# Optimization experiments

Measured on AMD Instinct MI355X. Metric: run time of the kernel, lower is better.

## Reference

```python
import jax, jax.numpy as jnp
import numpy as np

# Channel layout assumed by the model's CH dict
CH_ELEV, CH_WS, CH_WD, CH_HUM, CH_NDVI, CH_FIRE = 0, 1, 2, 3, 4, 5
P_BURN, W_WIND, W_SLOPE = 0.58, 0.045, 0.078
OFFSETS = [(-1, 0), (-1, 1), (0, 1), (1, 1), (1, 0), (1, -1), (0, -1), (-1, -1)]
DIR_ANGLES = [90.0, 45.0, 0.0, 315.0, 270.0, 225.0, 180.0, 135.0]
SOBEL_X = np.array([[-1, 0, 1], [-2, 0, 2], [-1, 0, 1]], np.float32) / 8.0
SOBEL_Y = np.array([[-1, -2, -1], [0, 0, 0], [1, 2, 1]], np.float32) / 8.0


def setup_inputs() -> dict:
    key = jax.random.key(0)
    x = jax.random.uniform(key, (16, 6, 1024, 1024), dtype=jnp.float32)
    return {"x": x}


def _conv2d_same(img, k):
    # img: (B,1,H,W), k: (3,3)
    kern = jnp.asarray(k).reshape(1, 1, 3, 3)
    return jax.lax.conv_general_dilated(img, kern, (1, 1), ((1, 1), (1, 1)))


def _shift(mask, dr, dc):
    # mask: (B,H,W) float; zero-padded shift matching torch slicing
    B, H, W = mask.shape
    p = jnp.pad(mask, ((0, 0), (1, 1), (1, 1)))
    return p[:, 1 + dr:1 + dr + H, 1 + dc:1 + dc + W]


def reference(x):
    B, C, H, W = x.shape
    elev = x[:, CH_ELEV:CH_ELEV + 1]          # (B,1,H,W)
    ws = x[:, CH_WS]                           # (B,H,W)
    wd = x[:, CH_WD]
    hum = x[:, CH_HUM]
    ndvi = x[:, CH_NDVI]
    fs = x[:, CH_FIRE]

    dx = _conv2d_same(elev, SOBEL_X)
    dy = _conv2d_same(elev, SOBEL_Y)
    grad_mag = jnp.sqrt(dx * dx + dy * dy + 1e-8)
    slope = (jnp.arctan(grad_mag) * (180.0 / np.pi))[:, 0]  # (B,H,W) degrees

    burning = (fs > 0.5).astype(x.dtype)
    wind_math = jnp.mod(270.0 - wd, 360.0)
    slope_effect = 1.0 + W_SLOPE * jnp.tan(slope * (np.pi / 180.0))
    moisture_damp = jnp.clip(1.0 - 2.0 * hum * 200.0, 0.3, 1.0)
    veg_factor = 0.5 + 0.5 * jnp.clip(ndvi, 0.0, 1.0)
    base = P_BURN * slope_effect * moisture_damp * veg_factor  # wind-independent part

    prob = jnp.zeros((B, H, W), dtype=x.dtype)
    for (dr, dc), d_angle in zip(OFFSETS, DIR_ANGLES):
        shifted = _shift(burning, dr, dc)
        angle_diff = (d_angle - wind_math) * (np.pi / 180.0)
        wind_factor = 1.0 + W_WIND * jnp.cos(angle_diff) * ws
        p_spread = jnp.clip(base * wind_factor, 0.0, 1.0)
        prob = jnp.maximum(prob, shifted * p_spread)

    unburned = (fs < 0.5).astype(x.dtype)
    out = jnp.maximum(fs, prob * unburned)
    return out[:, None]  # (B,1,H,W)
```

## Files before the change

### kernel.cpp

```cpp
#include <hip/hip_runtime.h>

namespace {
constexpr int CH = 6;
constexpr int H  = 1024;
constexpr int W  = 1024;
constexpr float P_BURN  = 0.58f;
constexpr float W_WIND  = 0.045f;
constexpr float W_SLOPE = 0.078f;
constexpr float C45     = 0.70710678118654752f;
constexpr float DEG2RAD = 0.017453292519943295f;

__device__ __forceinline__ void load6(const float* __restrict__ plane, int row,
                                      int j0, float v[6]) {
    if ((unsigned)row >= (unsigned)H) {
        v[0] = v[1] = v[2] = v[3] = v[4] = v[5] = 0.f;
        return;
    }
    const float* r = plane + (size_t)row * W;
    const float4 m = *reinterpret_cast<const float4*>(r + j0);
    v[0] = (j0 > 0)     ? r[j0 - 1] : 0.f;
    v[1] = m.x; v[2] = m.y; v[3] = m.z; v[4] = m.w;
    v[5] = (j0 + 4 < W) ? r[j0 + 4] : 0.f;
}
}

__global__ __launch_bounds__(256)
void fire_step(const float* __restrict__ x, float* __restrict__ out, int B) {
    const int nblk  = gridDim.x;
    const int chunk = nblk >> 3;
    const int bid   = blockIdx.x;
    const int srow  = (bid & 7) * chunk + (bid >> 3);

    const int b = srow / H;
    const int i = srow % H;
    if (b >= B) return;
    const int j0 = (int)threadIdx.x * 4;

    const size_t plane = (size_t)H * W;
    const float* base_b = x + (size_t)b * CH * plane;
    const float* elev  = base_b + 0 * plane;
    const float* wsp   = base_b + 1 * plane;
    const float* wdp   = base_b + 2 * plane;
    const float* hump  = base_b + 3 * plane;
    const float* ndvip = base_b + 4 * plane;
    const float* fsp   = base_b + 5 * plane;

    float em[6], ec[6], ep[6];
    load6(elev, i - 1, j0, em);
    load6(elev, i,     j0, ec);
    load6(elev, i + 1, j0, ep);
    float fm[6], fc[6], fq[6];
    load6(fsp, i - 1, j0, fm);
    load6(fsp, i,     j0, fc);
    load6(fsp, i + 1, j0, fq);

    const size_t roff = (size_t)i * W + j0;
    const float4 ws4 = *reinterpret_cast<const float4*>(wsp   + roff);
    const float4 wd4 = *reinterpret_cast<const float4*>(wdp   + roff);
    const float4 hu4 = *reinterpret_cast<const float4*>(hump  + roff);
    const float4 nd4 = *reinterpret_cast<const float4*>(ndvip + roff);
    const float* wsa = reinterpret_cast<const float*>(&ws4);
    const float* wda = reinterpret_cast<const float*>(&wd4);
    const float* hua = reinterpret_cast<const float*>(&hu4);
    const float* nda = reinterpret_cast<const float*>(&nd4);

    float o[4];
#pragma unroll
    for (int k = 0; k < 4; ++k) {
        const float dx = ((em[k+2] - em[k]) + 2.f * (ec[k+2] - ec[k]) +
                          (ep[k+2] - ep[k])) * 0.125f;
        const float dy = ((ep[k]   - em[k]) + 2.f * (ep[k+1] - em[k+1]) +
                          (ep[k+2] - em[k+2])) * 0.125f;
        const float g = sqrtf(dx * dx + dy * dy + 1e-8f);
        const float slope_eff = 1.f + W_SLOPE * g;
        const float moist = fminf(fmaxf(1.f - 400.f * hua[k], 0.3f), 1.f);
        const float veg   = 0.5f + 0.5f * fminf(fmaxf(nda[k], 0.f), 1.f);
        const float basep = P_BURN * slope_eff * moist * veg;

        const float wrad = (270.f - wda[k]) * DEG2RAD;
        float sw, cw;
        __sincosf(wrad, &sw, &cw);

        float best = -2.f;
        if (fm[k+1] > 0.5f) best = fmaxf(best,  sw);
        if (fm[k+2] > 0.5f) best = fmaxf(best,  C45 * (cw + sw));
        if (fc[k+2] > 0.5f) best = fmaxf(best,  cw);
        if (fq[k+2] > 0.5f) best = fmaxf(best,  C45 * (cw - sw));
        if (fq[k+1] > 0.5f) best = fmaxf(best, -sw);
        if (fq[k]   > 0.5f) best = fmaxf(best, -C45 * (cw + sw));
        if (fc[k]   > 0.5f) best = fmaxf(best, -cw);
        if (fm[k]   > 0.5f) best = fmaxf(best,  C45 * (sw - cw));

        float prob = 0.f;
        if (best > -1.5f) {
            const float wf = 1.f + W_WIND * best * wsa[k];
            prob = fminf(fmaxf(basep * wf, 0.f), 1.f);
        }
        const float fsc = fc[k + 1];
        o[k] = fmaxf(fsc, (fsc < 0.5f) ? prob : 0.f);
    }

    float4 ov;
    ov.x = o[0]; ov.y = o[1]; ov.z = o[2]; ov.w = o[3];
    *reinterpret_cast<float4*>(out + (size_t)b * plane + roff) = ov;
}

extern "C" void kernel_launch(void* const* d_in, const int* in_sizes, int n_in,
                              void* d_out, int out_size, void* d_ws, size_t ws_size,
                              hipStream_t stream) {
    const float* x = (const float*)d_in[0];
    float* out = (float*)d_out;
    const int B = in_sizes[0] / (CH * H * W);
    const int blocks = B * H;
    fire_step<<<blocks, 256, 0, stream>>>(x, out, B);
}
```

Measured before the change: 541.3 us.

## Tile elevation and fire planes into shared memory with 2D blocks

Replaces the one-row-per-block layout with 128x16 2D tiles. The elevation and fire-state halos are staged once in LDS and the 3x3 neighbourhoods are read from there, instead of each thread issuing redundant global loads for the neighbouring rows. It also drops the XCD-aware row swizzle. In exchange it adds a __syncthreads, halo overhead of 18 rows per 16 output rows, and about 20 KB of LDS per block, which may limit occupancy.

```diff
diff --git a/kernel.cpp b/kernel.cpp
--- a/kernel.cpp
+++ b/kernel.cpp
@@ -4,105 +4,143 @@
 constexpr int CH = 6;
 constexpr int H  = 1024;
 constexpr int W  = 1024;
+constexpr int TW = 128;
+constexpr int TH = 16;
+constexpr int LW = TW + 8;
+constexpr int LH = TH + 2;
 constexpr float P_BURN  = 0.58f;
 constexpr float W_WIND  = 0.045f;
 constexpr float W_SLOPE = 0.078f;
 constexpr float C45     = 0.70710678118654752f;
 constexpr float DEG2RAD = 0.017453292519943295f;
-
-__device__ __forceinline__ void load6(const float* __restrict__ plane, int row,
-                                      int j0, float v[6]) {
-    if ((unsigned)row >= (unsigned)H) {
-        v[0] = v[1] = v[2] = v[3] = v[4] = v[5] = 0.f;
-        return;
-    }
-    const float* r = plane + (size_t)row * W;
-    const float4 m = *reinterpret_cast<const float4*>(r + j0);
-    v[0] = (j0 > 0)     ? r[j0 - 1] : 0.f;
-    v[1] = m.x; v[2] = m.y; v[3] = m.z; v[4] = m.w;
-    v[5] = (j0 + 4 < W) ? r[j0 + 4] : 0.f;
-}
 }
 
 __global__ __launch_bounds__(256)
 void fire_step(const float* __restrict__ x, float* __restrict__ out, int B) {
-    const int nblk  = gridDim.x;
-    const int chunk = nblk >> 3;
-    const int bid   = blockIdx.x;
-    const int srow  = (bid & 7) * chunk + (bid >> 3);
+    __shared__ float es[LH][LW];
+    __shared__ float fs[LH][LW];
 
-    const int b = srow / H;
-    const int i = srow % H;
+    constexpr int tilesX = W / TW;
+    constexpr int tilesY = H / TH;
+    constexpr int tpi    = tilesX * tilesY;
+
+    const int b  = blockIdx.x / tpi;
+    const int t  = blockIdx.x % tpi;
+    const int r0 = (t / tilesX) * TH;
+    const int c0 = (t % tilesX) * TW;
     if (b >= B) return;
-    const int j0 = (int)threadIdx.x * 4;
 
     const size_t plane = (size_t)H * W;
-    const float* base_b = x + (size_t)b * CH * plane;
-    const float* elev  = base_b + 0 * plane;
-    const float* wsp   = base_b + 1 * plane;
-    const float* wdp   = base_b + 2 * plane;
-    const float* hump  = base_b + 3 * plane;
-    const float* ndvip = base_b + 4 * plane;
-    const float* fsp   = base_b + 5 * plane;
+    const float* bb    = x + (size_t)b * CH * plane;
+    const float* elev  = bb + 0 * plane;
+    const float* wsp   = bb + 1 * plane;
+    const float* wdp   = bb + 2 * plane;
+    const float* hup   = bb + 3 * plane;
+    const float* ndp   = bb + 4 * plane;
+    const float* fsp   = bb + 5 * plane;
 
-    float em[6], ec[6], ep[6];
-    load6(elev, i - 1, j0, em);
-    load6(elev, i,     j0, ec);
-    load6(elev, i + 1, j0, ep);
-    float fm[6], fc[6], fq[6];
-    load6(fsp, i - 1, j0, fm);
-    load6(fsp, i,     j0, fc);
-    load6(fsp, i + 1, j0, fq);
+    for (int idx = threadIdx.x; idx < LH * (LW / 4); idx += 256) {
+        const int lr = idx / (LW / 4);
+        const int g  = idx % (LW / 4);
+        const int gr = r0 - 1 + lr;
+        const int gc = c0 - 4 + 4 * g;
+        float4 e = {0.f, 0.f, 0.f, 0.f};
+        float4 f = {0.f, 0.f, 0.f, 0.f};
+        if ((unsigned)gr < (unsigned)H) {
+            const float* er = elev + (size_t)gr * W;
+            const float* fr = fsp  + (size_t)gr * W;
+            if (gc >= 0 && gc + 3 < W) {
+                e = *reinterpret_cast<const float4*>(er + gc);
+                f = *reinterpret_cast<const float4*>(fr + gc);
+            } else {
+                float* ep_ = reinterpret_cast<float*>(&e);
+                float* fp_ = reinterpret_cast<float*>(&f);
+#pragma unroll
+                for (int k = 0; k < 4; ++k) {
+                    const int c = gc + k;
+                    if ((unsigned)c < (unsigned)W) { ep_[k] = er[c]; fp_[k] = fr[c]; }
+                }
+            }
+        }
+        *reinterpret_cast<float4*>(&es[lr][4 * g]) = e;
+        *reinterpret_cast<float4*>(&fs[lr][4 * g]) = f;
+    }
+    __syncthreads();
 
-    const size_t roff = (size_t)i * W + j0;
-    const float4 ws4 = *reinterpret_cast<const float4*>(wsp   + roff);
-    const float4 wd4 = *reinterpret_cast<const float4*>(wdp   + roff);
-    const float4 hu4 = *reinterpret_cast<const float4*>(hump  + roff);
-    const float4 nd4 = *reinterpret_cast<const float4*>(ndvip + roff);
-    const float* wsa = reinterpret_cast<const float*>(&ws4);
-    const float* wda = reinterpret_cast<const float*>(&wd4);
-    const float* hua = reinterpret_cast<const float*>(&hu4);
-    const float* nda = reinterpret_cast<const float*>(&nd4);
+    const int tx = threadIdx.x & 31;
+    const int ty = threadIdx.x >> 5;
+    const int cbase = 4 * tx + 4;
 
-    float o[4];
+    auto rd6 = [&](const float (*sm)[LW], int r, float v[6]) {
+        const float4 mid = *reinterpret_cast<const float4*>(&sm[r][cbase]);
+        v[0] = sm[r][cbase - 1];
+        v[1] = mid.x; v[2] = mid.y; v[3] = mid.z; v[4] = mid.w;
+        v[5] = sm[r][cbase + 4];
+    };
+
 #pragma unroll
-    for (int k = 0; k < 4; ++k) {
-        const float dx = ((em[k+2] - em[k]) + 2.f * (ec[k+2] - ec[k]) +
-                          (ep[k+2] - ep[k])) * 0.125f;
-        const float dy = ((ep[k]   - em[k]) + 2.f * (ep[k+1] - em[k+1]) +
-                          (ep[k+2] - em[k+2])) * 0.125f;
-        const float g = sqrtf(dx * dx + dy * dy + 1e-8f);
-        const float slope_eff = 1.f + W_SLOPE * g;
-        const float moist = fminf(fmaxf(1.f - 400.f * hua[k], 0.3f), 1.f);
-        const float veg   = 0.5f + 0.5f * fminf(fmaxf(nda[k], 0.f), 1.f);
-        const float basep = P_BURN * slope_eff * moist * veg;
+    for (int s = 0; s < 2; ++s) {
+        const int lr = ty + 8 * s;
+        const int i  = r0 + lr;
+        const size_t roff = (size_t)i * W + c0 + 4 * tx;
 
-        const float wrad = (270.f - wda[k]) * DEG2RAD;
-        float sw, cw;
-        __sincosf(wrad, &sw, &cw);
+        const float4 ws4 = *reinterpret_cast<const float4*>(wsp + roff);
+        const float4 wd4 = *reinterpret_cast<const float4*>(wdp + roff);
+        const float4 hu4 = *reinterpret_cast<const float4*>(hup + roff);
+        const float4 nd4 = *reinterpret_cast<const float4*>(ndp + roff);
+        const float* wsa = reinterpret_cast<const float*>(&ws4);
+        const float* wda = reinterpret_cast<const float*>(&wd4);
+        const float* hua = reinterpret_cast<const float*>(&hu4);
+        const float* nda = reinterpret_cast<const float*>(&nd4);
 
-        float best = -2.f;
-        if (fm[k+1] > 0.5f) best = fmaxf(best,  sw);
-        if (fm[k+2] > 0.5f) best = fmaxf(best,  C45 * (cw + sw));
-        if (fc[k+2] > 0.5f) best = fmaxf(best,  cw);
-        if (fq[k+2] > 0.5f) best = fmaxf(best,  C45 * (cw - sw));
-        if (fq[k+1] > 0.5f) best = fmaxf(best, -sw);
-        if (fq[k]   > 0.5f) best = fmaxf(best, -C45 * (cw + sw));
-        if (fc[k]   > 0.5f) best = fmaxf(best, -cw);
-        if (fm[k]   > 0.5f) best = fmaxf(best,  C45 * (sw - cw));
+        float em[6], ec[6], ep[6], fm[6], fc[6], fq[6];
+        rd6(es, lr,     em);
+        rd6(es, lr + 1, ec);
+        rd6(es, lr + 2, ep);
+        rd6(fs, lr,     fm);
+        rd6(fs, lr + 1, fc);
+        rd6(fs, lr + 2, fq);
 
-        float prob = 0.f;
-        if (best > -1.5f) {
-            const float wf = 1.f + W_WIND * best * wsa[k];
-            prob = fminf(fmaxf(basep * wf, 0.f), 1.f);
+        float o[4];
+#pragma unroll
+        for (int k = 0; k < 4; ++k) {
+            const float dx = ((em[k+2] - em[k]) + 2.f * (ec[k+2] - ec[k]) +
+                              (ep[k+2] - ep[k])) * 0.125f;
+            const float dy = ((ep[k]   - em[k]) + 2.f * (ep[k+1] - em[k+1]) +
+                              (ep[k+2] - em[k+2])) * 0.125f;
+            const float g = sqrtf(dx * dx + dy * dy + 1e-8f);
+            const float slope_eff = 1.f + W_SLOPE * g;
+            const float moist = fminf(fmaxf(1.f - 400.f * hua[k], 0.3f), 1.f);
+            const float veg   = 0.5f + 0.5f * fminf(fmaxf(nda[k], 0.f), 1.f);
+            const float basep = P_BURN * slope_eff * moist * veg;
+
+            const float wrad = (270.f - wda[k]) * DEG2RAD;
+            float sw, cw;
+            __sincosf(wrad, &sw, &cw);
+
+            float best = -2.f;
+            if (fm[k+1] > 0.5f) best = fmaxf(best,  sw);
+            if (fm[k+2] > 0.5f) best = fmaxf(best,  C45 * (cw + sw));
+            if (fc[k+2] > 0.5f) best = fmaxf(best,  cw);
+            if (fq[k+2] > 0.5f) best = fmaxf(best,  C45 * (cw - sw));
+            if (fq[k+1] > 0.5f) best = fmaxf(best, -sw);
+            if (fq[k]   > 0.5f) best = fmaxf(best, -C45 * (cw + sw));
+            if (fc[k]   > 0.5f) best = fmaxf(best, -cw);
+            if (fm[k]   > 0.5f) best = fmaxf(best,  C45 * (sw - cw));
+
+            float prob = 0.f;
+            if (best > -1.5f) {
+                const float wf = 1.f + W_WIND * best * wsa[k];
+                prob = fminf(fmaxf(basep * wf, 0.f), 1.f);
+            }
+            const float fsc = fc[k + 1];
+            o[k] = fmaxf(fsc, (fsc < 0.5f) ? prob : 0.f);
         }
-        const float fsc = fc[k + 1];
-        o[k] = fmaxf(fsc, (fsc < 0.5f) ? prob : 0.f);
+
+        float4 ov;
+        ov.x = o[0]; ov.y = o[1]; ov.z = o[2]; ov.w = o[3];
+        *reinterpret_cast<float4*>(out + (size_t)b * plane + roff) = ov;
     }
-
-    float4 ov;
-    ov.x = o[0]; ov.y = o[1]; ov.z = o[2]; ov.w = o[3];
-    *reinterpret_cast<float4*>(out + (size_t)b * plane + roff) = ov;
 }
 
 extern "C" void kernel_launch(void* const* d_in, const int* in_sizes, int n_in,
@@ -111,6 +149,6 @@
     const float* x = (const float*)d_in[0];
     float* out = (float*)d_out;
     const int B = in_sizes[0] / (CH * H * W);
-    const int blocks = B * H;
+    const int blocks = B * (W / TW) * (H / TH);
     fire_step<<<blocks, 256, 0, stream>>>(x, out, B);
 }
```

New measurement: 533.9 us. About the same (-1.4%).
